# Optimization experiments

Hardware: AMD Instinct MI355X
Metric: run time of the kernel (lower is better)

## Reference

```python
import jax, jax.numpy as jnp
import numpy as np

B, S, D = 4, 2048, 2048
H, G, HD = 16, 4, 128  # n_heads, kv groups, head_dim
EPS = 1e-6


def setup_inputs() -> dict:
    key = jax.random.key(0)
    ks = jax.random.split(key, 8)
    x = jax.random.normal(ks[0], (B, S, D), dtype=jnp.float32)
    # causal mask, True = attend (already 'inverted' for SDPA semantics)
    mask = jnp.tril(jnp.ones((S, S), dtype=bool))
    # RoPE tables: (S, HD), rotate-half convention with duplicated freqs
    inv_freq = 1.0 / (10000.0 ** (np.arange(0, HD, 2, dtype=np.float32) / HD))
    ang = np.arange(S, dtype=np.float32)[:, None] * inv_freq[None, :]  # (S, HD/2)
    ang = np.concatenate([ang, ang], axis=-1)  # (S, HD)
    cos = jnp.asarray(np.cos(ang))
    sin = jnp.asarray(np.sin(ang))
    s = 0.02
    wq = jax.random.normal(ks[1], (D, H * HD), dtype=jnp.float32) * s
    wk = jax.random.normal(ks[2], (D, G * HD), dtype=jnp.float32) * s
    wv = jax.random.normal(ks[3], (D, G * HD), dtype=jnp.float32) * s
    wg = jax.random.normal(ks[4], (D, H * HD), dtype=jnp.float32) * s
    wo = jax.random.normal(ks[5], (H * HD, D), dtype=jnp.float32) * s
    q_scale = jax.random.normal(ks[6], (HD,), dtype=jnp.float32) * 0.01  # zero-centered
    k_scale = jax.random.normal(ks[7], (HD,), dtype=jnp.float32) * 0.01
    return dict(x=x, mask=mask, cos=cos, sin=sin, wq=wq, wk=wk, wv=wv,
                wg=wg, wo=wo, q_scale=q_scale, k_scale=k_scale)


def _zc_rmsnorm(x, scale):
    # zero-centered RMSNorm in fp32: x * rsqrt(mean(x^2)+eps) * (1+scale)
    xf = x.astype(jnp.float32)
    rms = jax.lax.rsqrt(jnp.mean(xf * xf, axis=-1, keepdims=True) + EPS)
    return (xf * rms * (1.0 + scale)).astype(x.dtype)


def _rope(x, cos, sin):
    # x: (b, h, s, hd); cos/sin: (s, hd)
    hd = x.shape[-1]
    x1, x2 = x[..., : hd // 2], x[..., hd // 2 :]
    rot = jnp.concatenate([-x2, x1], axis=-1)
    return x * cos[None, None] + rot * sin[None, None]


def reference(x, mask, cos, sin, wq, wk, wv, wg, wo, q_scale, k_scale):
    b, s, d = x.shape
    q = (x @ wq).reshape(b, s, H, HD).transpose(0, 2, 1, 3)   # (b,H,s,hd)
    k = (x @ wk).reshape(b, s, G, HD).transpose(0, 2, 1, 3)   # (b,G,s,hd)
    v = (x @ wv).reshape(b, s, G, HD).transpose(0, 2, 1, 3)
    gate = jax.nn.sigmoid(x @ wg)                              # (b,s,H*HD)

    q = _rope(_zc_rmsnorm(q, q_scale), cos, sin)
    k = _rope(_zc_rmsnorm(k, k_scale), cos, sin)

    rep = H // G
    k = jnp.repeat(k, rep, axis=1)   # (b,H,s,hd)
    v = jnpep = jnp.repeat(v, rep, axis=1) if False else jnp.repeat(v, rep, axis=1)

    scores = jnp.einsum('bhqd,bhkd->bhqk', q, k) / jnp.sqrt(jnp.float32(HD))
    scores = jnp.where(mask[None, None, :s, :s], scores, jnp.float32(-1e30))
    attn = jax.nn.softmax(scores, axis=-1)
    ctx = jnp.einsum('bhqk,bhkd->bhqd', attn, v)               # (b,H,s,hd)
    ctx = ctx.transpose(0, 2, 1, 3).reshape(b, s, H * HD)
    return (ctx * gate) @ wo
```

## Files before the change

kernel.cpp:

```cpp
#include <hip/hip_runtime.h>

typedef __bf16 bf16;
typedef __attribute__((ext_vector_type(8))) __bf16 bf16x8;
typedef __attribute__((ext_vector_type(4))) float f32x4;

constexpr int Bb = 4, S = 2048, Dd = 2048, H = 16, G = 4, HD = 128;
constexpr float L2E = 1.4426950408889634f;

__device__ inline f32x4 mfma16(bf16x8 a, bf16x8 b, f32x4 c) {
  return __builtin_amdgcn_mfma_f32_16x16x32_bf16(a, b, c, 0, 0, 0);
}

__device__ inline void gl_lds16(const void* g, void* l) {
  __builtin_amdgcn_global_load_lds(
      (const __attribute__((address_space(1))) void*)g,
      (__attribute__((address_space(3))) void*)l, 16, 0, 0);
}

__global__ __launch_bounds__(256) void k_f32_to_bf16(
    const float* __restrict__ in, bf16* __restrict__ out, int n8) {
  int i = blockIdx.x * 256 + threadIdx.x;
  if (i >= n8) return;
  const float4* p = (const float4*)(in + (long long)i * 8);
  float4 a = p[0], b = p[1];
  bf16x8 v;
  v[0] = (bf16)a.x; v[1] = (bf16)a.y; v[2] = (bf16)a.z; v[3] = (bf16)a.w;
  v[4] = (bf16)b.x; v[5] = (bf16)b.y; v[6] = (bf16)b.z; v[7] = (bf16)b.w;
  *(bf16x8*)(out + (long long)i * 8) = v;
}

template <typename InT>
__global__ __launch_bounds__(256) void k_transpose_bf16(
    const InT* __restrict__ in, long long s1, int nb2, long long s2, int ldin,
    bf16* __restrict__ out, long long obatch, int ldout, int R, int C) {
  __shared__ float tile[32][33];
  int z = blockIdx.z;
  const InT* ip = in + (long long)(z / nb2) * s1 + (long long)(z % nb2) * s2;
  bf16* op = out + (long long)z * obatch;
  int c0 = blockIdx.x * 32, r0 = blockIdx.y * 32;
  int tx = threadIdx.x, ty = threadIdx.y;
#pragma unroll
  for (int i = 0; i < 4; ++i) {
    int r = r0 + ty + i * 8, c = c0 + tx;
    tile[ty + i * 8][tx] = (r < R && c < C) ? (float)ip[(long long)r * ldin + c] : 0.f;
  }
  __syncthreads();
#pragma unroll
  for (int i = 0; i < 4; ++i) {
    int c = c0 + ty + i * 8, r = r0 + tx;
    if (c < C && r < R) op[(long long)c * ldout + r] = (bf16)tile[tx][ty + i * 8];
  }
}

template <typename CT>
__global__ __launch_bounds__(512, 2) void k_gemm256(
    const bf16* __restrict__ A, int lda, const bf16* __restrict__ Bt, int ldb,
    CT* __restrict__ C, int ldc, int M, int N, int K) {
  __shared__ bf16 ldsbuf[65536];
  char* lds2 = (char*)ldsbuf;
  const int tid = threadIdx.x;
  const int w = tid >> 6, lane = tid & 63;
  const int l16 = lane & 15, lh = lane >> 4;
  const int wr = w >> 2, wc = w & 3;
  const int nbn = N >> 8;
  const int cpx = gridDim.x >> 3;
  const int swz = (blockIdx.x & 7) * cpx + (blockIdx.x >> 3);
  const int bm = swz / nbn, bn = swz % nbn;
  const int m0 = bm << 8, n0 = bn << 8;

  const int lrow = lane >> 3;
  const int lcol = ((lane & 7) ^ lrow) * 8;
  const int arb = wr * 128 + wc * 16;
  const int xg = wc >> 1, sg = wr * 2 + (wc & 1);
  const int brb = xg * 128 + (sg >> 1) * 64 + (sg & 1) * 16;
  const bf16* aS0 = A + (long long)(m0 + arb + lrow) * lda + lcol;
  const bf16* aS1 = A + (long long)(m0 + arb + 8 + lrow) * lda + lcol;
  const bf16* bS0 = Bt + (long long)(n0 + brb + lrow) * ldb + lcol;
  const bf16* bS1 = Bt + (long long)(n0 + brb + 8 + lrow) * ldb + lcol;

  auto stageA = [&](int buf, int k0, int hi) {
    gl_lds16(aS0 + (long long)hi * 64 * lda + k0,
             lds2 + buf * 65536 + (arb + hi * 64) * 128);
    gl_lds16(aS1 + (long long)hi * 64 * lda + k0,
             lds2 + buf * 65536 + (arb + hi * 64 + 8) * 128);
  };
  auto stageB = [&](int buf, int k0, int hi) {
    gl_lds16(bS0 + (long long)hi * 32 * ldb + k0,
             lds2 + buf * 65536 + 32768 + (brb + hi * 32) * 128);
    gl_lds16(bS1 + (long long)hi * 32 * ldb + k0,
             lds2 + buf * 65536 + 32768 + (brb + hi * 32 + 8) * 128);
  };

  f32x4 acc[8][4] = {};
  const int NT = K >> 6;

  stageA(0, 0, 0);
  stageB(0, 0, 0);
  stageB(0, 0, 1);
  stageA(0, 0, 1);
  asm volatile("s_waitcnt vmcnt(4)" ::: "memory");
  __builtin_amdgcn_s_barrier();

  const int swzc = (l16 & 7) << 4;
  for (int t = 0; t < NT; ++t) {
    const int buf = t & 1, nb = buf ^ 1;
    const int kn = (t + 1) << 6;
    const bool more = (t + 1 < NT);
    const char* La = lds2 + buf * 65536;
    const char* Lb = La + 32768;
    bf16x8 af[4][2], bn0[2][2], bn1[2][2];
    if (more) stageA(nb, kn, 0);
#pragma unroll
    for (int m = 0; m < 4; ++m)
#pragma unroll
      for (int ks = 0; ks < 2; ++ks)
        af[m][ks] = *(const bf16x8*)(La + (wr * 128 + m * 16 + l16) * 128 +
                                     ((ks * 64 + lh * 16) ^ swzc));
#pragma unroll
    for (int n = 0; n < 2; ++n)
#pragma unroll
      for (int ks = 0; ks < 2; ++ks)
        bn0[n][ks] = *(const bf16x8*)(Lb + (wc * 64 + n * 16 + l16) * 128 +
                                      ((ks * 64 + lh * 16) ^ swzc));
    __builtin_amdgcn_s_barrier();
    asm volatile("s_waitcnt lgkmcnt(0)" ::: "memory");
    __builtin_amdgcn_sched_barrier(0);
    __builtin_amdgcn_s_setprio(1);
#pragma unroll
    for (int m = 0; m < 4; ++m)
#pragma unroll
      for (int n = 0; n < 2; ++n)
#pragma unroll
        for (int ks = 0; ks < 2; ++ks)
          acc[m][n] = mfma16(af[m][ks], bn0[n][ks], acc[m][n]);
    __builtin_amdgcn_s_setprio(0);
    asm volatile("s_waitcnt vmcnt(4)" ::: "memory");
    __builtin_amdgcn_s_barrier();
    if (more) stageB(nb, kn, 0);
#pragma unroll
    for (int n = 0; n < 2; ++n)
#pragma unroll
      for (int ks = 0; ks < 2; ++ks)
        bn1[n][ks] = *(const bf16x8*)(Lb + (wc * 64 + 32 + n * 16 + l16) * 128 +
                                      ((ks * 64 + lh * 16) ^ swzc));
    __builtin_amdgcn_s_barrier();
    asm volatile("s_waitcnt lgkmcnt(0)" ::: "memory");
    __builtin_amdgcn_sched_barrier(0);
    __builtin_amdgcn_s_setprio(1);
#pragma unroll
    for (int m = 0; m < 4; ++m)
#pragma unroll
      for (int n = 0; n < 2; ++n)
#pragma unroll
        for (int ks = 0; ks < 2; ++ks)
          acc[m][2 + n] = mfma16(af[m][ks], bn1[n][ks], acc[m][2 + n]);
    __builtin_amdgcn_s_setprio(0);
    asm volatile("s_waitcnt vmcnt(4)" ::: "memory");
    __builtin_amdgcn_s_barrier();
    if (more) stageB(nb, kn, 1);
#pragma unroll
    for (int m = 0; m < 4; ++m)
#pragma unroll
      for (int ks = 0; ks < 2; ++ks)
        af[m][ks] = *(const bf16x8*)(La + (wr * 128 + 64 + m * 16 + l16) * 128 +
                                     ((ks * 64 + lh * 16) ^ swzc));
    __builtin_amdgcn_s_barrier();
    asm volatile("s_waitcnt lgkmcnt(0)" ::: "memory");
    __builtin_amdgcn_sched_barrier(0);
    __builtin_amdgcn_s_setprio(1);
#pragma unroll
    for (int m = 0; m < 4; ++m)
#pragma unroll
      for (int n = 0; n < 2; ++n)
#pragma unroll
        for (int ks = 0; ks < 2; ++ks)
          acc[4 + m][2 + n] = mfma16(af[m][ks], bn1[n][ks], acc[4 + m][2 + n]);
    __builtin_amdgcn_s_setprio(0);
    __builtin_amdgcn_s_barrier();
    if (more) stageA(nb, kn, 1);
    __builtin_amdgcn_s_barrier();
    __builtin_amdgcn_s_setprio(1);
#pragma unroll
    for (int m = 0; m < 4; ++m)
#pragma unroll
      for (int n = 0; n < 2; ++n)
#pragma unroll
        for (int ks = 0; ks < 2; ++ks)
          acc[4 + m][n] = mfma16(af[m][ks], bn0[n][ks], acc[4 + m][n]);
    __builtin_amdgcn_s_setprio(0);
    asm volatile("s_waitcnt vmcnt(4)" ::: "memory");
    __builtin_amdgcn_s_barrier();
  }

#pragma unroll
  for (int m = 0; m < 8; ++m)
#pragma unroll
    for (int n = 0; n < 4; ++n)
#pragma unroll
      for (int r = 0; r < 4; ++r)
        C[(long long)(m0 + wr * 128 + m * 16 + lh * 4 + r) * ldc + n0 + wc * 64 +
          n * 16 + l16] = (CT)acc[m][n][r];
}

__global__ __launch_bounds__(256) void k_rms_rope(
    const bf16* __restrict__ in, int ldin, int nh, const float* __restrict__ scale,
    const float* __restrict__ cosT, const float* __restrict__ sinT,
    bf16* __restrict__ out, float oscale, int nwaves) {
  int wid = (blockIdx.x * 256 + threadIdx.x) >> 6;
  if (wid >= nwaves) return;
  int lane = threadIdx.x & 63;
  int h = wid % nh;
  int bs = wid / nh;
  int s = bs % S;
  int b = bs / S;
  const bf16* ip = in + (long long)bs * ldin + h * HD;
  float x1 = (float)ip[lane], x2 = (float)ip[lane + 64];
  float ss = x1 * x1 + x2 * x2;
#pragma unroll
  for (int m = 1; m < 64; m <<= 1) ss += __shfl_xor(ss, m);
  float rms = rsqrtf(ss * (1.f / 128.f) + 1e-6f);
  float n1 = x1 * rms * (1.f + scale[lane]);
  float n2 = x2 * rms * (1.f + scale[lane + 64]);
  float o1 = (n1 * cosT[s * 128 + lane] - n2 * sinT[s * 128 + lane]) * oscale;
  float o2 = (n2 * cosT[s * 128 + lane + 64] + n1 * sinT[s * 128 + lane + 64]) * oscale;
  bf16* op = out + (((long long)b * nh + h) * S + s) * HD;
  op[lane] = (bf16)o1;
  op[lane + 64] = (bf16)o2;
}

__global__ __launch_bounds__(256) void k_sigmoid(bf16* __restrict__ p, int ld,
                                                 int cols8, int n) {
  int i = blockIdx.x * 256 + threadIdx.x;
  if (i >= n) return;
  int row = i / cols8, c = (i % cols8) * 8;
  bf16x8* q = (bf16x8*)(p + (long long)row * ld + c);
  bf16x8 v = *q;
#pragma unroll
  for (int j = 0; j < 8; ++j) {
    float f = (float)v[j];
    v[j] = (bf16)(1.f / (1.f + exp2f(-f * L2E)));
  }
  *q = v;
}

__global__ __launch_bounds__(512, 2) void k_flash3(
    const bf16* __restrict__ Q, const bf16* __restrict__ Kb,
    const bf16* __restrict__ Vt, const bf16* __restrict__ gate, int ldg,
    bf16* __restrict__ outc, int ldo) {
  __shared__ bf16 Ks[2][64 * 128];
  __shared__ bf16 Vs[128 * 64];
  __shared__ bf16 Ps[8][32 * 64];
  const int tid = threadIdx.x, w = tid >> 6, lane = tid & 63;
  const int l16 = lane & 15, lh = lane >> 4;
  const int bh = blockIdx.x & 63;
  const int qi = blockIdx.x >> 6;
  const int qc = 7 - qi;
  const int h = bh & 15, b = bh >> 4, g = h >> 2;
  const int qbase = qc * 256;
  const int q0w = qbase + w * 32;
  const bf16* qp = Q + (((long long)b * H + h) * S + q0w) * HD;
  const bf16* kp = Kb + ((long long)b * G + g) * S * HD;
  const bf16* vp = Vt + ((long long)b * G + g) * (long long)HD * S;

  bf16x8 aq[2][4];
#pragma unroll
  for (int m = 0; m < 2; ++m)
#pragma unroll
    for (int ks = 0; ks < 4; ++ks)
      aq[m][ks] = *(const bf16x8*)(qp + (long long)(m * 16 + l16) * HD + ks * 32 + lh * 8);

  f32x4 acc[2][8] = {};
  float mrow[2][4], lrow[2][4];
#pragma unroll
  for (int m = 0; m < 2; ++m)
#pragma unroll
    for (int r = 0; r < 4; ++r) { mrow[m][r] = -1e30f; lrow[m][r] = 0.f; }

  const int ntiles = qc * 4 + 4;

  auto stageK = [&](int bi, int t) {
    const int kv0 = t << 6;
#pragma unroll
    for (int i = 0; i < 2; ++i) {
      int c = w * 128 + i * 64 + lane;
      int row = c >> 4;
      int cb = ((c & 15) << 4) ^ ((row & 7) << 4);
      gl_lds16(kp + (long long)(kv0 + row) * HD + (cb >> 1),
               (char*)Ks[bi] + (w * 128 + i * 64) * 16);
    }
  };
  auto stageV = [&](int t) {
    const int kv0 = t << 6;
#pragma unroll
    for (int i = 0; i < 2; ++i) {
      int c = w * 128 + i * 64 + lane;
      int rowv = c >> 3;
      int cbv = ((c & 7) << 4) ^ ((rowv & 7) << 4);
      gl_lds16(vp + (long long)rowv * S + kv0 + (cbv >> 1),
               (char*)Vs + (w * 128 + i * 64) * 16);
    }
  };

  stageK(0, 0);
  asm volatile("s_waitcnt vmcnt(0)" ::: "memory");
  __builtin_amdgcn_s_barrier();
  asm volatile("" ::: "memory");

  for (int t = 0; t < ntiles; ++t) {
    const int buf = t & 1;
    const int kv0 = t << 6;
    const bool active = (kv0 <= q0w + 31);
    stageV(t);
    if (t + 1 < ntiles) stageK(buf ^ 1, t + 1);
    if (active) {
      f32x4 s[2][4] = {};
#pragma unroll
      for (int ks = 0; ks < 4; ++ks)
#pragma unroll
        for (int n = 0; n < 4; ++n) {
          int row = n * 16 + l16;
          int off = row * 256 + ((ks * 64 + lh * 16) ^ ((row & 7) << 4));
          bf16x8 kb = *(const bf16x8*)((const char*)Ks[buf] + off);
#pragma unroll
          for (int m = 0; m < 2; ++m) s[m][n] = mfma16(aq[m][ks], kb, s[m][n]);
        }
      if (kv0 + 63 > q0w) {
#pragma unroll
        for (int m = 0; m < 2; ++m)
#pragma unroll
          for (int n = 0; n < 4; ++n)
#pragma unroll
            for (int r = 0; r < 4; ++r) {
              int col = kv0 + n * 16 + l16;
              int rowg = q0w + m * 16 + lh * 4 + r;
              if (col > rowg) s[m][n][r] = -1e30f;
            }
      }
      float lm[2][4];
      bool okl = true;
#pragma unroll
      for (int m = 0; m < 2; ++m)
#pragma unroll
        for (int r = 0; r < 4; ++r) {
          lm[m][r] = fmaxf(fmaxf(s[m][0][r], s[m][1][r]), fmaxf(s[m][2][r], s[m][3][r]));
          okl = okl && (lm[m][r] <= mrow[m][r] + 8.f);
        }
      if (!__all(okl)) {
#pragma unroll
        for (int st = 1; st < 16; st <<= 1)
#pragma unroll
          for (int m = 0; m < 2; ++m)
#pragma unroll
            for (int r = 0; r < 4; ++r) lm[m][r] = fmaxf(lm[m][r], __shfl_xor(lm[m][r], st));
#pragma unroll
        for (int m = 0; m < 2; ++m)
#pragma unroll
          for (int r = 0; r < 4; ++r) {
            float mn = fmaxf(mrow[m][r], lm[m][r]);
            float resc = exp2f(mrow[m][r] - mn);
            mrow[m][r] = mn;
            lrow[m][r] *= resc;
#pragma unroll
            for (int dt = 0; dt < 8; ++dt) acc[m][dt][r] *= resc;
          }
      }
#pragma unroll
      for (int m = 0; m < 2; ++m)
#pragma unroll
        for (int n = 0; n < 4; ++n)
#pragma unroll
          for (int r = 0; r < 4; ++r) {
            float p = exp2f(s[m][n][r] - mrow[m][r]);
            s[m][n][r] = p;
            int row = m * 16 + lh * 4 + r;
            *(bf16*)((char*)Ps[w] + row * 128 +
                     ((n * 32 + l16 * 2) ^ ((row & 7) << 4))) = (bf16)p;
          }
#pragma unroll
      for (int m = 0; m < 2; ++m)
#pragma unroll
        for (int r = 0; r < 4; ++r)
          lrow[m][r] += s[m][0][r] + s[m][1][r] + s[m][2][r] + s[m][3][r];
    }
    asm volatile("s_waitcnt vmcnt(2)" ::: "memory");
    __builtin_amdgcn_s_barrier();
    asm volatile("" ::: "memory");
    if (active) {
      bf16x8 pa[2][2];
#pragma unroll
      for (int m = 0; m < 2; ++m)
#pragma unroll
        for (int kf = 0; kf < 2; ++kf) {
          int row = m * 16 + l16;
          pa[m][kf] = *(const bf16x8*)((const char*)Ps[w] + row * 128 +
                                       ((kf * 64 + lh * 16) ^ ((row & 7) << 4)));
        }
#pragma unroll
      for (int dt = 0; dt < 8; ++dt) {
        int d = dt * 16 + l16;
#pragma unroll
        for (int kf = 0; kf < 2; ++kf) {
          int off = d * 128 + ((kf * 64 + lh * 16) ^ ((d & 7) << 4));
          bf16x8 vb = *(const bf16x8*)((const char*)Vs + off);
#pragma unroll
          for (int m = 0; m < 2; ++m) acc[m][dt] = mfma16(pa[m][kf], vb, acc[m][dt]);
        }
      }
    }
    asm volatile("s_waitcnt vmcnt(0)" ::: "memory");
    __builtin_amdgcn_s_barrier();
    asm volatile("" ::: "memory");
  }

#pragma unroll
  for (int st = 1; st < 16; st <<= 1)
#pragma unroll
    for (int m = 0; m < 2; ++m)
#pragma unroll
      for (int r = 0; r < 4; ++r) lrow[m][r] += __shfl_xor(lrow[m][r], st);
  float inv[2][4];
#pragma unroll
  for (int m = 0; m < 2; ++m)
#pragma unroll
    for (int r = 0; r < 4; ++r) inv[m][r] = 1.f / lrow[m][r];
#pragma unroll
  for (int m = 0; m < 2; ++m)
#pragma unroll
    for (int dt = 0; dt < 8; ++dt)
#pragma unroll
      for (int r = 0; r < 4; ++r) {
        int rowg = q0w + m * 16 + lh * 4 + r;
        long long row = (long long)b * S + rowg;
        int col = h * HD + dt * 16 + l16;
        float gv = (float)gate[row * ldg + col];
        outc[row * ldo + col] = (bf16)(acc[m][dt][r] * inv[m][r] * gv);
      }
}

extern "C" void kernel_launch(void* const* d_in, const int* in_sizes, int n_in,
                              void* d_out, int out_size, void* d_ws, size_t ws_size,
                              hipStream_t stream) {
  const float* x = (const float*)d_in[0];
  const float* cosT = (const float*)d_in[2];
  const float* sinT = (const float*)d_in[3];
  const float* wq = (const float*)d_in[4];
  const float* wk = (const float*)d_in[5];
  const float* wv = (const float*)d_in[6];
  const float* wg = (const float*)d_in[7];
  const float* wo = (const float*)d_in[8];
  const float* qs = (const float*)d_in[9];
  const float* ksc = (const float*)d_in[10];
  float* out = (float*)d_out;
  char* ws = (char*)d_ws;

  if (ws_size < 146800640) return;
  bf16* xb = (bf16*)(ws);
  bf16* wcat = (bf16*)(ws + 33554432);
  bf16* woT = (bf16*)(ws + 54525952);
  bf16* C1 = (bf16*)(ws + 62914560);
  bf16* qbuf = xb;
  bf16* kbuf = wcat;
  bf16* vtbuf = wcat + 4194304;
  bf16* gatep = C1 + 3072;
  bf16* ctxg = C1;

  dim3 tb(32, 8);
  k_f32_to_bf16<<<8192, 256, 0, stream>>>(x, xb, Bb * S * Dd / 8);
  k_transpose_bf16<float><<<dim3(64, 64, 1), tb, 0, stream>>>(
      wq, 0, 1, 0, 2048, wcat, 0, 2048, 2048, 2048);
  k_transpose_bf16<float><<<dim3(16, 64, 1), tb, 0, stream>>>(
      wk, 0, 1, 0, 512, wcat + 2048 * 2048, 0, 2048, 2048, 512);
  k_transpose_bf16<float><<<dim3(16, 64, 1), tb, 0, stream>>>(
      wv, 0, 1, 0, 512, wcat + 2560 * 2048, 0, 2048, 2048, 512);
  k_transpose_bf16<float><<<dim3(64, 64, 1), tb, 0, stream>>>(
      wg, 0, 1, 0, 2048, wcat + 3072 * 2048, 0, 2048, 2048, 2048);
  k_transpose_bf16<float><<<dim3(64, 64, 1), tb, 0, stream>>>(
      wo, 0, 1, 0, 2048, woT, 0, 2048, 2048, 2048);
  k_gemm256<bf16><<<32 * 20, 512, 0, stream>>>(xb, 2048, wcat, 2048, C1, 5120,
                                               8192, 5120, 2048);
  k_rms_rope<<<32768, 256, 0, stream>>>(C1, 5120, 16, qs, cosT, sinT, qbuf,
                                        0.12751879523209308f, 131072);
  k_rms_rope<<<8192, 256, 0, stream>>>(C1 + 2048, 5120, 4, ksc, cosT, sinT, kbuf,
                                       1.0f, 32768);
  k_transpose_bf16<bf16><<<dim3(4, 64, 16), tb, 0, stream>>>(
      C1 + 2560, (long long)2048 * 5120, 4, 128, 5120, vtbuf,
      (long long)128 * 2048, 2048, 2048, 128);
  k_sigmoid<<<8192, 256, 0, stream>>>(gatep, 5120, 256, 2097152);
  k_flash3<<<512, 512, 0, stream>>>(qbuf, kbuf, vtbuf, gatep, 5120, ctxg, 5120);
  k_gemm256<float><<<32 * 8, 512, 0, stream>>>(ctxg, 5120, woT, 2048, out, 2048,
                                               8192, 2048, 2048);
}
```

Before: 478.9 us.

## Restructure GEMM pipeline, fuse sigmoid epilogue, merge weight transposes and rms-rope launches

The GEMM main loop is rescheduled so that LDS fragment reads for the next step are prefetched into registers while MFMAs run. This removes the lgkmcnt waits and several barriers per iteration, and launch bounds are relaxed to one block per SM to give the extra fragment registers room. The gate sigmoid is folded into the QKVG GEMM epilogue, which drops a separate read-modify-write pass. The five weight transposes are merged into one launch, and the q/k rms-rope kernels are merged into one launch, cutting launch overhead. Risks include lower occupancy and correctness of the rotated double-buffer staging, which clamps out-of-range k0 back to zero.

```diff
diff --git a/kernel.cpp b/kernel.cpp
--- a/kernel.cpp
+++ b/kernel.cpp
@@ -29,6 +29,39 @@
   *(bf16x8*)(out + (long long)i * 8) = v;
 }
 
+__global__ __launch_bounds__(256) void k_wtrans(
+    const float* __restrict__ wq, const float* __restrict__ wk,
+    const float* __restrict__ wv, const float* __restrict__ wg,
+    const float* __restrict__ wo, bf16* __restrict__ wcat,
+    bf16* __restrict__ woT) {
+  __shared__ float tile[32][33];
+  const int z = blockIdx.z;
+  const float* src;
+  bf16* dst;
+  int C;
+  switch (z) {
+    case 0: src = wq; C = 2048; dst = wcat; break;
+    case 1: src = wk; C = 512; dst = wcat + (long long)2048 * 2048; break;
+    case 2: src = wv; C = 512; dst = wcat + (long long)2560 * 2048; break;
+    case 3: src = wg; C = 2048; dst = wcat + (long long)3072 * 2048; break;
+    default: src = wo; C = 2048; dst = woT; break;
+  }
+  int c0 = blockIdx.x * 32, r0 = blockIdx.y * 32;
+  if (c0 >= C) return;
+  int tx = threadIdx.x, ty = threadIdx.y;
+#pragma unroll
+  for (int i = 0; i < 4; ++i) {
+    int r = r0 + ty + i * 8, c = c0 + tx;
+    tile[ty + i * 8][tx] = (c < C) ? src[(long long)r * C + c] : 0.f;
+  }
+  __syncthreads();
+#pragma unroll
+  for (int i = 0; i < 4; ++i) {
+    int c = c0 + ty + i * 8, r = r0 + tx;
+    if (c < C) dst[(long long)c * 2048 + r] = (bf16)tile[tx][ty + i * 8];
+  }
+}
+
 template <typename InT>
 __global__ __launch_bounds__(256) void k_transpose_bf16(
     const InT* __restrict__ in, long long s1, int nb2, long long s2, int ldin,
@@ -52,10 +85,10 @@
   }
 }
 
-template <typename CT>
-__global__ __launch_bounds__(512, 2) void k_gemm256(
+template <typename CT, bool SIG>
+__global__ __launch_bounds__(512, 1) void k_gemm256(
     const bf16* __restrict__ A, int lda, const bf16* __restrict__ Bt, int ldb,
-    CT* __restrict__ C, int ldc, int M, int N, int K) {
+    CT* __restrict__ C, int ldc, int M, int N, int K, int sig_from) {
   __shared__ bf16 ldsbuf[65536];
   char* lds2 = (char*)ldsbuf;
   const int tid = threadIdx.x;
@@ -79,73 +112,87 @@
   const bf16* bS1 = Bt + (long long)(n0 + brb + 8 + lrow) * ldb + lcol;
 
   auto stageA = [&](int buf, int k0, int hi) {
+    k0 = (k0 < K) ? k0 : 0;
     gl_lds16(aS0 + (long long)hi * 64 * lda + k0,
              lds2 + buf * 65536 + (arb + hi * 64) * 128);
     gl_lds16(aS1 + (long long)hi * 64 * lda + k0,
              lds2 + buf * 65536 + (arb + hi * 64 + 8) * 128);
   };
   auto stageB = [&](int buf, int k0, int hi) {
+    k0 = (k0 < K) ? k0 : 0;
     gl_lds16(bS0 + (long long)hi * 32 * ldb + k0,
              lds2 + buf * 65536 + 32768 + (brb + hi * 32) * 128);
     gl_lds16(bS1 + (long long)hi * 32 * ldb + k0,
              lds2 + buf * 65536 + 32768 + (brb + hi * 32 + 8) * 128);
   };
 
+  const int swzc = (l16 & 7) << 4;
+  auto rdA = [&](bf16x8 (&dst)[4][2], const char* L, int mh) {
+#pragma unroll
+    for (int m = 0; m < 4; ++m)
+#pragma unroll
+      for (int ks = 0; ks < 2; ++ks)
+        dst[m][ks] = *(const bf16x8*)(L + (wr * 128 + mh * 64 + m * 16 + l16) * 128 +
+                                      ((ks * 64 + lh * 16) ^ swzc));
+  };
+  auto rdB = [&](bf16x8 (&dst)[2][2], const char* L, int nh) {
+#pragma unroll
+    for (int n = 0; n < 2; ++n)
+#pragma unroll
+      for (int ks = 0; ks < 2; ++ks)
+        dst[n][ks] = *(const bf16x8*)(L + 32768 + (wc * 64 + nh * 32 + n * 16 + l16) * 128 +
+                                      ((ks * 64 + lh * 16) ^ swzc));
+  };
+
   f32x4 acc[8][4] = {};
+  bf16x8 aflo[4][2], afhi[4][2], bn0[2][2], bn1[2][2];
   const int NT = K >> 6;
 
   stageA(0, 0, 0);
   stageB(0, 0, 0);
   stageB(0, 0, 1);
   stageA(0, 0, 1);
+  stageA(1, 64, 0);
   asm volatile("s_waitcnt vmcnt(4)" ::: "memory");
   __builtin_amdgcn_s_barrier();
-
-  const int swzc = (l16 & 7) << 4;
+  asm volatile("" ::: "memory");
+  rdA(aflo, lds2, 0);
+  rdB(bn0, lds2, 0);
+
   for (int t = 0; t < NT; ++t) {
     const int buf = t & 1, nb = buf ^ 1;
-    const int kn = (t + 1) << 6;
+    const char* L = lds2 + buf * 65536;
+    const char* Ln = lds2 + nb * 65536;
+    const int k1 = (t + 1) << 6;
     const bool more = (t + 1 < NT);
-    const char* La = lds2 + buf * 65536;
-    const char* Lb = La + 32768;
-    bf16x8 af[4][2], bn0[2][2], bn1[2][2];
-    if (more) stageA(nb, kn, 0);
+    stageB(nb, k1, 0);
+    rdB(bn1, L, 1);
+    __builtin_amdgcn_s_setprio(1);
 #pragma unroll
     for (int m = 0; m < 4; ++m)
 #pragma unroll
-      for (int ks = 0; ks < 2; ++ks)
-        af[m][ks] = *(const bf16x8*)(La + (wr * 128 + m * 16 + l16) * 128 +
-                                     ((ks * 64 + lh * 16) ^ swzc));
-#pragma unroll
-    for (int n = 0; n < 2; ++n)
-#pragma unroll
-      for (int ks = 0; ks < 2; ++ks)
-        bn0[n][ks] = *(const bf16x8*)(Lb + (wc * 64 + n * 16 + l16) * 128 +
-                                      ((ks * 64 + lh * 16) ^ swzc));
-    __builtin_amdgcn_s_barrier();
-    asm volatile("s_waitcnt lgkmcnt(0)" ::: "memory");
-    __builtin_amdgcn_sched_barrier(0);
-    __builtin_amdgcn_s_setprio(1);
-#pragma unroll
-    for (int m = 0; m < 4; ++m)
-#pragma unroll
       for (int n = 0; n < 2; ++n)
 #pragma unroll
         for (int ks = 0; ks < 2; ++ks)
-          acc[m][n] = mfma16(af[m][ks], bn0[n][ks], acc[m][n]);
+          acc[m][n] = mfma16(aflo[m][ks], bn0[n][ks], acc[m][n]);
     __builtin_amdgcn_s_setprio(0);
     asm volatile("s_waitcnt vmcnt(4)" ::: "memory");
     __builtin_amdgcn_s_barrier();
-    if (more) stageB(nb, kn, 0);
-#pragma unroll
-    for (int n = 0; n < 2; ++n)
-#pragma unroll
-      for (int ks = 0; ks < 2; ++ks)
-        bn1[n][ks] = *(const bf16x8*)(Lb + (wc * 64 + 32 + n * 16 + l16) * 128 +
-                                      ((ks * 64 + lh * 16) ^ swzc));
+    asm volatile("" ::: "memory");
+    stageB(nb, k1, 1);
+    rdA(afhi, L, 1);
+    __builtin_amdgcn_s_setprio(1);
+#pragma unroll
+    for (int m = 0; m < 4; ++m)
+#pragma unroll
+      for (int n = 0; n < 2; ++n)
+#pragma unroll
+        for (int ks = 0; ks < 2; ++ks)
+          acc[m][2 + n] = mfma16(aflo[m][ks], bn1[n][ks], acc[m][2 + n]);
+    __builtin_amdgcn_s_setprio(0);
     __builtin_amdgcn_s_barrier();
-    asm volatile("s_waitcnt lgkmcnt(0)" ::: "memory");
-    __builtin_amdgcn_sched_barrier(0);
+    asm volatile("" ::: "memory");
+    stageA(nb, k1, 1);
     __builtin_amdgcn_s_setprio(1);
 #pragma unroll
     for (int m = 0; m < 4; ++m)
@@ -153,67 +200,72 @@
       for (int n = 0; n < 2; ++n)
 #pragma unroll
         for (int ks = 0; ks < 2; ++ks)
-          acc[m][2 + n] = mfma16(af[m][ks], bn1[n][ks], acc[m][2 + n]);
+          acc[4 + m][2 + n] = mfma16(afhi[m][ks], bn1[n][ks], acc[4 + m][2 + n]);
     __builtin_amdgcn_s_setprio(0);
     asm volatile("s_waitcnt vmcnt(4)" ::: "memory");
     __builtin_amdgcn_s_barrier();
-    if (more) stageB(nb, kn, 1);
+    asm volatile("" ::: "memory");
+    if (more) rdA(aflo, Ln, 0);
+    stageA(buf, (t + 2) << 6, 0);
+    __builtin_amdgcn_s_setprio(1);
 #pragma unroll
     for (int m = 0; m < 4; ++m)
 #pragma unroll
-      for (int ks = 0; ks < 2; ++ks)
-        af[m][ks] = *(const bf16x8*)(La + (wr * 128 + 64 + m * 16 + l16) * 128 +
-                                     ((ks * 64 + lh * 16) ^ swzc));
-    __builtin_amdgcn_s_barrier();
-    asm volatile("s_waitcnt lgkmcnt(0)" ::: "memory");
-    __builtin_amdgcn_sched_barrier(0);
-    __builtin_amdgcn_s_setprio(1);
-#pragma unroll
-    for (int m = 0; m < 4; ++m)
-#pragma unroll
       for (int n = 0; n < 2; ++n)
 #pragma unroll
         for (int ks = 0; ks < 2; ++ks)
-          acc[4 + m][2 + n] = mfma16(af[m][ks], bn1[n][ks], acc[4 + m][2 + n]);
+          acc[4 + m][n] = mfma16(afhi[m][ks], bn0[n][ks], acc[4 + m][n]);
     __builtin_amdgcn_s_setprio(0);
-    __builtin_amdgcn_s_barrier();
-    if (more) stageA(nb, kn, 1);
-    __builtin_amdgcn_s_barrier();
-    __builtin_amdgcn_s_setprio(1);
-#pragma unroll
-    for (int m = 0; m < 4; ++m)
-#pragma unroll
-      for (int n = 0; n < 2; ++n)
-#pragma unroll
-        for (int ks = 0; ks < 2; ++ks)
-          acc[4 + m][n] = mfma16(af[m][ks], bn0[n][ks], acc[4 + m][n]);
-    __builtin_amdgcn_s_setprio(0);
+    if (more) rdB(bn0, Ln, 0);
     asm volatile("s_waitcnt vmcnt(4)" ::: "memory");
     __builtin_amdgcn_s_barrier();
+    asm volatile("" ::: "memory");
   }
 
 #pragma unroll
   for (int m = 0; m < 8; ++m)
 #pragma unroll
-    for (int n = 0; n < 4; ++n)
-#pragma unroll
-      for (int r = 0; r < 4; ++r)
-        C[(long long)(m0 + wr * 128 + m * 16 + lh * 4 + r) * ldc + n0 + wc * 64 +
-          n * 16 + l16] = (CT)acc[m][n][r];
-}
-
-__global__ __launch_bounds__(256) void k_rms_rope(
-    const bf16* __restrict__ in, int ldin, int nh, const float* __restrict__ scale,
-    const float* __restrict__ cosT, const float* __restrict__ sinT,
-    bf16* __restrict__ out, float oscale, int nwaves) {
+    for (int n = 0; n < 4; ++n) {
+      const int col = n0 + wc * 64 + n * 16 + l16;
+#pragma unroll
+      for (int r = 0; r < 4; ++r) {
+        float v = acc[m][n][r];
+        if (SIG && col >= sig_from) v = 1.f / (1.f + exp2f(-v * L2E));
+        C[(long long)(m0 + wr * 128 + m * 16 + lh * 4 + r) * ldc + col] = (CT)v;
+      }
+    }
+}
+
+__global__ __launch_bounds__(256) void k_rms_rope2(
+    const bf16* __restrict__ C1, const float* __restrict__ qs,
+    const float* __restrict__ ksc, const float* __restrict__ cosT,
+    const float* __restrict__ sinT, bf16* __restrict__ qb,
+    bf16* __restrict__ kb) {
   int wid = (blockIdx.x * 256 + threadIdx.x) >> 6;
-  if (wid >= nwaves) return;
   int lane = threadIdx.x & 63;
-  int h = wid % nh;
-  int bs = wid / nh;
-  int s = bs % S;
-  int b = bs / S;
-  const bf16* ip = in + (long long)bs * ldin + h * HD;
+  const bf16* ip;
+  const float* scale;
+  bf16* op;
+  float oscale;
+  int s;
+  if (wid < 131072) {
+    int h = wid & 15, bs = wid >> 4;
+    s = bs & 2047;
+    int b = bs >> 11;
+    ip = C1 + (long long)bs * 5120 + h * HD;
+    scale = qs;
+    oscale = 0.12751879523209308f;
+    op = qb + (((long long)b * H + h) * S + s) * HD;
+  } else {
+    wid -= 131072;
+    int h = wid & 3, bs = wid >> 2;
+    s = bs & 2047;
+    int b = bs >> 11;
+    ip = C1 + 2048 + (long long)bs * 5120 + h * HD;
+    scale = ksc;
+    oscale = 1.0f;
+    op = kb + (((long long)b * G + h) * S + s) * HD;
+  }
   float x1 = (float)ip[lane], x2 = (float)ip[lane + 64];
   float ss = x1 * x1 + x2 * x2;
 #pragma unroll
@@ -223,24 +275,8 @@
   float n2 = x2 * rms * (1.f + scale[lane + 64]);
   float o1 = (n1 * cosT[s * 128 + lane] - n2 * sinT[s * 128 + lane]) * oscale;
   float o2 = (n2 * cosT[s * 128 + lane + 64] + n1 * sinT[s * 128 + lane + 64]) * oscale;
-  bf16* op = out + (((long long)b * nh + h) * S + s) * HD;
   op[lane] = (bf16)o1;
   op[lane + 64] = (bf16)o2;
-}
-
-__global__ __launch_bounds__(256) void k_sigmoid(bf16* __restrict__ p, int ld,
-                                                 int cols8, int n) {
-  int i = blockIdx.x * 256 + threadIdx.x;
-  if (i >= n) return;
-  int row = i / cols8, c = (i % cols8) * 8;
-  bf16x8* q = (bf16x8*)(p + (long long)row * ld + c);
-  bf16x8 v = *q;
-#pragma unroll
-  for (int j = 0; j < 8; ++j) {
-    float f = (float)v[j];
-    v[j] = (bf16)(1.f / (1.f + exp2f(-f * L2E)));
-  }
-  *q = v;
 }
 
 __global__ __launch_bounds__(512, 2) void k_flash3(
@@ -466,27 +502,14 @@
 
   dim3 tb(32, 8);
   k_f32_to_bf16<<<8192, 256, 0, stream>>>(x, xb, Bb * S * Dd / 8);
-  k_transpose_bf16<float><<<dim3(64, 64, 1), tb, 0, stream>>>(
-      wq, 0, 1, 0, 2048, wcat, 0, 2048, 2048, 2048);
-  k_transpose_bf16<float><<<dim3(16, 64, 1), tb, 0, stream>>>(
-      wk, 0, 1, 0, 512, wcat + 2048 * 2048, 0, 2048, 2048, 512);
-  k_transpose_bf16<float><<<dim3(16, 64, 1), tb, 0, stream>>>(
-      wv, 0, 1, 0, 512, wcat + 2560 * 2048, 0, 2048, 2048, 512);
-  k_transpose_bf16<float><<<dim3(64, 64, 1), tb, 0, stream>>>(
-      wg, 0, 1, 0, 2048, wcat + 3072 * 2048, 0, 2048, 2048, 2048);
-  k_transpose_bf16<float><<<dim3(64, 64, 1), tb, 0, stream>>>(
-      wo, 0, 1, 0, 2048, woT, 0, 2048, 2048, 2048);
-  k_gemm256<bf16><<<32 * 20, 512, 0, stream>>>(xb, 2048, wcat, 2048, C1, 5120,
-                                               8192, 5120, 2048);
-  k_rms_rope<<<32768, 256, 0, stream>>>(C1, 5120, 16, qs, cosT, sinT, qbuf,
-                                        0.12751879523209308f, 131072);
-  k_rms_rope<<<8192, 256, 0, stream>>>(C1 + 2048, 5120, 4, ksc, cosT, sinT, kbuf,
-                                       1.0f, 32768);
+  k_wtrans<<<dim3(64, 64, 5), tb, 0, stream>>>(wq, wk, wv, wg, wo, wcat, woT);
+  k_gemm256<bf16, true><<<32 * 20, 512, 0, stream>>>(
+      xb, 2048, wcat, 2048, C1, 5120, 8192, 5120, 2048, 3072);
+  k_rms_rope2<<<40960, 256, 0, stream>>>(C1, qs, ksc, cosT, sinT, qbuf, kbuf);
   k_transpose_bf16<bf16><<<dim3(4, 64, 16), tb, 0, stream>>>(
       C1 + 2560, (long long)2048 * 5120, 4, 128, 5120, vtbuf,
       (long long)128 * 2048, 2048, 2048, 128);
-  k_sigmoid<<<8192, 256, 0, stream>>>(gatep, 5120, 256, 2097152);
   k_flash3<<<512, 512, 0, stream>>>(qbuf, kbuf, vtbuf, gatep, 5120, ctxg, 5120);
-  k_gemm256<float><<<32 * 8, 512, 0, stream>>>(ctxg, 5120, woT, 2048, out, 2048,
-                                               8192, 2048, 2048);
-}
+  k_gemm256<float, false><<<32 * 8, 512, 0, stream>>>(
+      ctxg, 5120, woT, 2048, out, 2048, 8192, 2048, 2048, 1 << 30);
+}
```

Result: faster. 441.2 us (-7.9%).
